# Kernel optimization log

Hardware: AMD Instinct MI355X
Metric: run time of the kernel (lower is better)

The kernel has to match this reference:

```python
import jax, jax.numpy as jnp
import numpy as np

ENC_STRIDES = [1, 2, 4, 8, 16, 32, 64, 128]
POST_STRIDES = [1, 2, 4, 8, 16, 32]
NHEAD = 4
EPS = 1e-5


def _fsmn(x, lw, lb, mw, mb, stride):
    # h = Linear(x); memory[i] = MemLinear(mean(x[:, max(0,i-stride):i+1]))
    # Sliding-window mean via cumsum trick (vectorizes the per-timestep loop).
    h = x @ lw.T + lb
    L = x.shape[1]
    cs = jnp.cumsum(x, axis=1)                                   # [B,L,D]
    cs0 = jnp.concatenate([jnp.zeros_like(cs[:, :1]), cs], axis=1)  # [B,L+1,D]
    idx = jnp.arange(L)
    start = jnp.maximum(0, idx - stride)
    counts = (idx + 1 - start).astype(x.dtype)
    means = (cs - cs0[:, start]) / counts[None, :, None]
    return h + means @ mw.T + mb


def _ln(x, w, b):
    m = x.mean(-1, keepdims=True)
    v = ((x - m) ** 2).mean(-1, keepdims=True)
    return (x - m) / jnp.sqrt(v + EPS) * w + b


def _mha(x, in_w, in_b, out_w, out_b):
    B, L, D = x.shape
    hd = D // NHEAD
    qkv = x @ in_w.T + in_b                       # [B,L,3D]
    q, k, v = jnp.split(qkv, 3, axis=-1)
    sp = lambda t: t.reshape(B, L, NHEAD, hd).transpose(0, 2, 1, 3)
    q, k, v = sp(q), sp(k), sp(v)
    scores = jnp.einsum('bhld,bhmd->bhlm', q, k) / jnp.sqrt(jnp.asarray(hd, x.dtype))
    att = jax.nn.softmax(scores, axis=-1)
    o = jnp.einsum('bhlm,bhmd->bhld', att, v).transpose(0, 2, 1, 3).reshape(B, L, D)
    return o @ out_w.T + out_b


def _forward(x, speaker_embeddings,
             enc0_in_w, enc0_in_b, enc_lin_w, enc_lin_b, enc_mem_w, enc_mem_b,
             spk_w1, spk_b1, spk_w2, spk_b2, spk_w3, spk_b3,
             tr_in_w, tr_in_b, tr_out_w, tr_out_b, tr_ln1_w, tr_ln1_b,
             tr_ff1_w, tr_ff1_b, tr_ff2_w, tr_ff2_b, tr_ln2_w, tr_ln2_b,
             adapter_w, adapter_b, post_lin_w, post_lin_b, post_mem_w, post_mem_b,
             cls_w1, cls_b1, cls_w2, cls_b2):
    # speech encoder: 8 FSMN layers (layer 0 has an input projection 80->512)
    h = x @ enc0_in_w.T + enc0_in_b
    for i in range(8):
        h = _fsmn(h, enc_lin_w[i], enc_lin_b[i], enc_mem_w[i], enc_mem_b[i], ENC_STRIDES[i])
    # speaker encoder MLP (dropout = identity in eval)
    sf = jax.nn.relu(speaker_embeddings @ spk_w1.T + spk_b1)
    sf = jax.nn.relu(sf @ spk_w2.T + spk_b2)
    sf = sf @ spk_w3.T + spk_b3                   # [B,S,D]
    # context-independent scores: [B,L,S]
    ci = jnp.einsum('bld,bsd->bls', h, sf)
    # context-dependent scorer: 4-layer post-norm transformer encoder (relu FFN)
    cd = h
    for i in range(4):
        a = _mha(cd, tr_in_w[i], tr_in_b[i], tr_out_w[i], tr_out_b[i])
        cd = _ln(cd + a, tr_ln1_w[i], tr_ln1_b[i])
        f = jax.nn.relu(cd @ tr_ff1_w[i].T + tr_ff1_b[i]) @ tr_ff2_w[i].T + tr_ff2_b[i]
        cd = _ln(cd + f, tr_ln2_w[i], tr_ln2_b[i])
    comb = jnp.concatenate([ci, cd], axis=2) @ adapter_w.T + adapter_b  # [B,L,D]
    for i in range(6):
        comb = _fsmn(comb, post_lin_w[i], post_lin_b[i], post_mem_w[i], post_mem_b[i], POST_STRIDES[i])
    out = jax.nn.relu(comb @ cls_w1.T + cls_b1) @ cls_w2.T + cls_b2
    return out


def setup_inputs() -> dict:
    B, L, F, D, S, C = 8, 2048, 80, 512, 4, 16
    key = jax.random.key(0)
    ks = iter(jax.random.split(key, 64))
    p = lambda shape, s=0.02: jax.random.normal(next(ks), shape, jnp.float32) * s
    inp = {
        'x': jax.random.normal(next(ks), (B, L, F), jnp.float32),
        'speaker_embeddings': jax.random.normal(next(ks), (B, S, 192), jnp.float32),
        'enc0_in_w': p((D, F)), 'enc0_in_b': p((D,)),
        'enc_lin_w': p((8, D, D)), 'enc_lin_b': p((8, D)),
        'enc_mem_w': p((8, D, D)), 'enc_mem_b': p((8, D)),
        'spk_w1': p((D, 192)), 'spk_b1': p((D,)),
        'spk_w2': p((D, D)), 'spk_b2': p((D,)),
        'spk_w3': p((D, D)), 'spk_b3': p((D,)),
        'tr_in_w': p((4, 3 * D, D)), 'tr_in_b': p((4, 3 * D)),
        'tr_out_w': p((4, D, D)), 'tr_out_b': p((4, D)),
        'tr_ln1_w': jnp.ones((4, D), jnp.float32), 'tr_ln1_b': jnp.zeros((4, D), jnp.float32),
        'tr_ff1_w': p((4, 4 * D, D)), 'tr_ff1_b': p((4, 4 * D)),
        'tr_ff2_w': p((4, D, 4 * D)), 'tr_ff2_b': p((4, D)),
        'tr_ln2_w': jnp.ones((4, D), jnp.float32), 'tr_ln2_b': jnp.zeros((4, D), jnp.float32),
        'adapter_w': p((D, S + D)), 'adapter_b': p((D,)),
        'post_lin_w': p((6, D, D)), 'post_lin_b': p((6, D)),
        'post_mem_w': p((6, D, D)), 'post_mem_b': p((6, D)),
        'cls_w1': p((D, D)), 'cls_b1': p((D,)),
        'cls_w2': p((C, D)), 'cls_b2': p((C,)),
    }
    return inp


def reference(x, speaker_embeddings,
              enc0_in_w, enc0_in_b, enc_lin_w, enc_lin_b, enc_mem_w, enc_mem_b,
              spk_w1, spk_b1, spk_w2, spk_b2, spk_w3, spk_b3,
              tr_in_w, tr_in_b, tr_out_w, tr_out_b, tr_ln1_w, tr_ln1_b,
              tr_ff1_w, tr_ff1_b, tr_ff2_w, tr_ff2_b, tr_ln2_w, tr_ln2_b,
              adapter_w, adapter_b, post_lin_w, post_lin_b, post_mem_w, post_mem_b,
              cls_w1, cls_b1, cls_w2, cls_b2):
    return _forward(x, speaker_embeddings,
                    enc0_in_w, enc0_in_b, enc_lin_w, enc_lin_b, enc_mem_w, enc_mem_b,
                    spk_w1, spk_b1, spk_w2, spk_b2, spk_w3, spk_b3,
                    tr_in_w, tr_in_b, tr_out_w, tr_out_b, tr_ln1_w, tr_ln1_b,
                    tr_ff1_w, tr_ff1_b, tr_ff2_w, tr_ff2_b, tr_ln2_w, tr_ln2_b,
                    adapter_w, adapter_b, post_lin_w, post_lin_b, post_mem_w, post_mem_b,
                    cls_w1, cls_b1, cls_w2, cls_b2)
```

## Files before the change

kernel.cpp:

```cpp
#include <hip/hip_runtime.h>
#include <hip/hip_bf16.h>
#include <math.h>

typedef unsigned short u16t;
using f32x4 = __attribute__((ext_vector_type(4))) float;
using s16x8 = __attribute__((ext_vector_type(8))) short;
using us8   = __attribute__((ext_vector_type(8))) unsigned short;

#define GB_RELU 1
#define GB_WF32 4
#define GB_WB16 8

__device__ __forceinline__ u16t f2b(float f) {
    unsigned u = __float_as_uint(f);
    unsigned r = (u + 0x7FFFu + ((u >> 16) & 1u)) >> 16;
    return (u16t)r;
}
__device__ __forceinline__ float b2f(u16t s) {
    return __uint_as_float(((unsigned)s) << 16);
}
__device__ __forceinline__ void gload16(const void* gsrc, void* ldst) {
    __builtin_amdgcn_global_load_lds(
        (const __attribute__((address_space(1))) void*)gsrc,
        (__attribute__((address_space(3))) void*)ldst, 16, 0, 0);
}

__global__ __launch_bounds__(512)
void gemm_bf16(const u16t* __restrict__ A, int lda,
               const u16t* __restrict__ W, int ldw,
               const float* __restrict__ bias,
               float* __restrict__ C, int ldc,
               u16t* __restrict__ Cb, int ldcb,
               int M, int N, int K, int flags)
{
    __shared__ u16t SM[32768];
    u16t* As = SM;
    u16t* Ws = SM + 16384;
    const int tid = threadIdx.x;
    const int lane = tid & 63, w = tid >> 6;
    const int wr = w >> 2, wc = w & 3;
    const int l15 = lane & 15, l4 = lane >> 4;

    unsigned nwg = gridDim.x * gridDim.y;
    unsigned bid = blockIdx.y * gridDim.x + blockIdx.x;
    if ((nwg & 7u) == 0u) bid = (bid & 7u) * (nwg >> 3) + (bid >> 3);
    const int m0 = (int)(bid / gridDim.x) * 128;
    const int n0 = (int)(bid % gridDim.x) * 128;

    int arow[2], wrow[2], koff[2], se0[2];
#pragma unroll
    for (int it = 0; it < 2; ++it) {
        const int e = it * 512 + tid;
        se0[it] = it * 512 + (tid & 448);
        const int kb = e >> 7, r = e & 127;
        const int rg = r ^ (kb & 3);
        int gm = m0 + rg; if (gm > M - 1) gm = M - 1;
        arow[it] = gm;
        wrow[it] = n0 + rg;
        koff[it] = kb * 8;
    }

    f32x4 acc[4][2];
#pragma unroll
    for (int i = 0; i < 4; ++i)
#pragma unroll
        for (int j = 0; j < 2; ++j) acc[i][j] = (f32x4){0.f, 0.f, 0.f, 0.f};

    auto STAGE = [&](int buf, int k0) {
#pragma unroll
        for (int it = 0; it < 2; ++it)
            gload16(A + (size_t)arow[it] * lda + k0 + koff[it],
                    &As[(size_t)(buf * 8192 + se0[it] * 8)]);
#pragma unroll
        for (int it = 0; it < 2; ++it)
            gload16(W + (size_t)wrow[it] * ldw + k0 + koff[it],
                    &Ws[(size_t)(buf * 8192 + se0[it] * 8)]);
    };

    const int nk = K >> 6;
    STAGE(0, 0);
    for (int ks = 0; ks < nk; ++ks) {
        const int cur = ks & 1;
        if (ks + 1 < nk) {
            STAGE(cur ^ 1, (ks + 1) << 6);
            asm volatile("s_waitcnt vmcnt(4)" ::: "memory");
        } else {
            asm volatile("s_waitcnt vmcnt(0)" ::: "memory");
        }
        __builtin_amdgcn_s_barrier();
#pragma unroll
        for (int kk = 0; kk < 2; ++kk) {
            const int kb = kk * 4 + l4;
            const int ls = l15 ^ l4;
            s16x8 a[4], b[2];
#pragma unroll
            for (int mi = 0; mi < 4; ++mi)
                a[mi] = *(const s16x8*)&As[(size_t)(cur * 8192 + (kb * 128 + wr * 64 + mi * 16 + ls) * 8)];
#pragma unroll
            for (int ni = 0; ni < 2; ++ni)
                b[ni] = *(const s16x8*)&Ws[(size_t)(cur * 8192 + (kb * 128 + wc * 32 + ni * 16 + ls) * 8)];
#pragma unroll
            for (int mi = 0; mi < 4; ++mi)
#pragma unroll
                for (int ni = 0; ni < 2; ++ni)
                    acc[mi][ni] = __builtin_amdgcn_mfma_f32_16x16x32_bf16(
                        a[mi], b[ni], acc[mi][ni], 0, 0, 0);
        }
        __builtin_amdgcn_s_barrier();
    }

    if (flags & GB_WB16) __syncthreads();
#pragma unroll
    for (int mi = 0; mi < 4; ++mi) {
#pragma unroll
        for (int r = 0; r < 4; ++r) {
            const int rowl = wr * 64 + mi * 16 + l4 * 4 + r;
            const int row = m0 + rowl;
            const bool rok = row < M;
#pragma unroll
            for (int ni = 0; ni < 2; ++ni) {
                const int coll = wc * 32 + ni * 16 + l15;
                float v = acc[mi][ni][r];
                if (bias) v += bias[n0 + coll];
                if (flags & GB_RELU) v = fmaxf(v, 0.f);
                if ((flags & GB_WF32) && rok) C[(size_t)row * ldc + n0 + coll] = v;
                if (flags & GB_WB16) SM[rowl * 136 + coll] = f2b(v);
            }
        }
    }
    if (flags & GB_WB16) {
        __syncthreads();
#pragma unroll
        for (int rr = 0; rr < 4; ++rr) {
            const int rowl = rr * 32 + (tid >> 4);
            const int c0 = (tid & 15) * 8;
            if (m0 + rowl < M)
                *(us8*)(Cb + (size_t)(m0 + rowl) * ldcb + n0 + c0) =
                    *(const us8*)&SM[rowl * 136 + c0];
        }
    }
}

__global__ __launch_bounds__(256)
void fsmn_means_b(u16t* __restrict__ HM, int stride)
{
    const int d = blockIdx.x * 256 + threadIdx.x;
    const int b = blockIdx.z;
    const int c0 = blockIdx.y * 128;
    const u16t* Hp = HM + (size_t)b * 2048 * 1024 + d;
    u16t* Mp = HM + (size_t)b * 2048 * 1024 + 512 + d;
    float sum = 0.f;
    int s0 = c0 - stride; if (s0 < 0) s0 = 0;
    for (int j = s0; j < c0; ++j) sum += b2f(Hp[(size_t)j * 1024]);
    for (int i = c0; i < c0 + 128; ++i) {
        sum += b2f(Hp[(size_t)i * 1024]);
        const int st = i - stride;
        const float cnt = (float)(i + 1 - (st > 0 ? st : 0));
        Mp[(size_t)i * 1024] = f2b(sum / cnt);
        if (st >= 0) sum -= b2f(Hp[(size_t)st * 1024]);
    }
}

__global__ __launch_bounds__(256)
void ci_kernel(const u16t* __restrict__ HM, const float* __restrict__ SF,
               float* __restrict__ CI)
{
    const int idx = blockIdx.x * 256 + threadIdx.x;
    const int s = idx & 3;
    const int bl = idx >> 2;
    const int b = bl >> 11;
    const us8* h8 = (const us8*)(HM + (size_t)bl * 1024);
    const float4* f4 = (const float4*)(SF + ((size_t)(b * 4 + s)) * 512);
    float acc = 0.f;
    for (int k = 0; k < 64; ++k) {
        const us8 hv = h8[k];
        const float4 f0 = f4[k * 2], f1 = f4[k * 2 + 1];
        acc += b2f(hv[0]) * f0.x + b2f(hv[1]) * f0.y + b2f(hv[2]) * f0.z + b2f(hv[3]) * f0.w
             + b2f(hv[4]) * f1.x + b2f(hv[5]) * f1.y + b2f(hv[6]) * f1.z + b2f(hv[7]) * f1.w;
    }
    CI[idx] = acc;
}

__global__ __launch_bounds__(256)
void ln_add_f32(const float* __restrict__ X, const float* __restrict__ R,
                const float* __restrict__ w, const float* __restrict__ b,
                float* __restrict__ Y, u16t* __restrict__ Yb)
{
    const int lane = threadIdx.x & 63, wid = threadIdx.x >> 6;
    const size_t row = (size_t)blockIdx.x * 4 + wid;
    const float* x = X + row * 512;
    const float* r = R + row * 512;
    const int c0 = lane * 8;
    float v[8];
    {
        const float4 a0 = *(const float4*)(x + c0);
        const float4 a1 = *(const float4*)(x + c0 + 4);
        const float4 r0 = *(const float4*)(r + c0);
        const float4 r1 = *(const float4*)(r + c0 + 4);
        v[0] = a0.x + r0.x; v[1] = a0.y + r0.y; v[2] = a0.z + r0.z; v[3] = a0.w + r0.w;
        v[4] = a1.x + r1.x; v[5] = a1.y + r1.y; v[6] = a1.z + r1.z; v[7] = a1.w + r1.w;
    }
    float s = 0.f;
#pragma unroll
    for (int j = 0; j < 8; ++j) s += v[j];
#pragma unroll
    for (int off = 1; off < 64; off <<= 1) s += __shfl_xor(s, off);
    const float mean = s * (1.f / 512.f);
    float q = 0.f;
#pragma unroll
    for (int j = 0; j < 8; ++j) { const float dd = v[j] - mean; q += dd * dd; }
#pragma unroll
    for (int off = 1; off < 64; off <<= 1) q += __shfl_xor(q, off);
    const float rstd = rsqrtf(q * (1.f / 512.f) + 1e-5f);
    float* y = Y + row * 512;
    u16t* yb = Yb + row * 1024;
#pragma unroll
    for (int j = 0; j < 8; ++j) {
        const float o = (v[j] - mean) * rstd * w[c0 + j] + b[c0 + j];
        y[c0 + j] = o;
        yb[c0 + j] = f2b(o);
    }
}

__global__ __launch_bounds__(256)
void vtprep(const u16t* __restrict__ QKVb, u16t* __restrict__ Vt)
{
    __shared__ u16t T[128 * 72];
    const int tid = threadIdx.x;
    const int l0 = blockIdx.x * 64;
    const int bh = blockIdx.y, b = bh >> 2, h = bh & 3;
#pragma unroll
    for (int it = 0; it < 4; ++it) {
        const int e = it * 256 + tid;
        const int l = e >> 4, dc = e & 15;
        const us8 v = *(const us8*)(QKVb + ((size_t)(b * 2048 + l0 + l)) * 1536
                                   + 1024 + h * 128 + dc * 8);
#pragma unroll
        for (int j = 0; j < 8; ++j) T[(dc * 8 + j) * 72 + l] = v[j];
    }
    __syncthreads();
#pragma unroll
    for (int it = 0; it < 4; ++it) {
        const int e = it * 256 + tid;
        const int d = e >> 3, lc = e & 7;
        const us8 ov = *(const us8*)&T[d * 72 + lc * 8];
        *(us8*)(Vt + ((size_t)bh * 128 + d) * 2048 + l0 + lc * 8) = ov;
    }
}

__global__ __launch_bounds__(512)
void attn_bf16(const u16t* __restrict__ QKVb, const u16t* __restrict__ Vt,
               u16t* __restrict__ AOb)
{
    __shared__ u16t Kt[2][8192];
    __shared__ u16t Vtl[2][8192];
    __shared__ u16t Pl[8192];
    const int tid = threadIdx.x, lane = tid & 63, w = tid >> 6;
    const int l15 = lane & 15, l4 = lane >> 4;
    const unsigned bid = blockIdx.y * gridDim.x + blockIdx.x;
    const int xcd = bid & 7, idx = bid >> 3;
    const int bh = xcd * 4 + (idx & 3);
    const int q0 = (idx >> 2) * 128;
    const int b = bh >> 2, h = bh & 3;
    const float SCALE = 0.08838834764831845f;

    int krow[2], kdoff[2], vd[2], vkoff[2], se0[2];
#pragma unroll
    for (int it = 0; it < 2; ++it) {
        const int e = it * 512 + tid;
        se0[it] = it * 512 + (tid & 448);
        const int dblk = e >> 6, key = e & 63;
        krow[it] = key ^ (dblk & 3);
        kdoff[it] = dblk * 8;
        const int kb = e >> 7, d = e & 127;
        vd[it] = d ^ (kb & 3);
        vkoff[it] = kb * 8;
    }
    auto STAGE = [&](int buf, int k0) {
#pragma unroll
        for (int it = 0; it < 2; ++it)
            gload16(QKVb + ((size_t)(b * 2048 + k0 + krow[it])) * 1536 + 512 + h * 128 + kdoff[it],
                    &Kt[buf][(size_t)se0[it] * 8]);
#pragma unroll
        for (int it = 0; it < 2; ++it)
            gload16(Vt + ((size_t)bh * 128 + vd[it]) * 2048 + k0 + vkoff[it],
                    &Vtl[buf][(size_t)se0[it] * 8]);
    };

    s16x8 qf[4];
    {
        const u16t* qp = QKVb + ((size_t)(b * 2048 + q0 + w * 16 + l15)) * 1536
                         + h * 128 + l4 * 8;
#pragma unroll
        for (int ks = 0; ks < 4; ++ks) qf[ks] = *(const s16x8*)(qp + ks * 32);
    }
    asm volatile("s_waitcnt vmcnt(0)" ::: "memory");

    f32x4 o[8];
#pragma unroll
    for (int i = 0; i < 8; ++i) o[i] = (f32x4){0.f, 0.f, 0.f, 0.f};
    f32x4 m_run, lsum;
#pragma unroll
    for (int r = 0; r < 4; ++r) { m_run[r] = -1e30f; lsum[r] = 0.f; }

    const int ls = l15 ^ l4;
    STAGE(0, 0);
    for (int kt = 0; kt < 32; ++kt) {
        const int cur = kt & 1;
        if (kt + 1 < 32) {
            STAGE(cur ^ 1, (kt + 1) * 64);
            asm volatile("s_waitcnt vmcnt(4)" ::: "memory");
        } else {
            asm volatile("s_waitcnt vmcnt(0)" ::: "memory");
        }
        __builtin_amdgcn_s_barrier();

        f32x4 s[4];
#pragma unroll
        for (int ni = 0; ni < 4; ++ni) s[ni] = (f32x4){0.f, 0.f, 0.f, 0.f};
#pragma unroll
        for (int ks = 0; ks < 4; ++ks) {
#pragma unroll
            for (int ni = 0; ni < 4; ++ni) {
                const s16x8 kf = *(const s16x8*)&Kt[cur][(size_t)((ks * 4 + l4) * 64 + ni * 16 + ls) * 8];
                s[ni] = __builtin_amdgcn_mfma_f32_16x16x32_bf16(qf[ks], kf, s[ni], 0, 0, 0);
            }
        }
        f32x4 mx;
#pragma unroll
        for (int r = 0; r < 4; ++r)
            mx[r] = fmaxf(fmaxf(s[0][r], s[1][r]), fmaxf(s[2][r], s[3][r])) * SCALE;
#pragma unroll
        for (int off = 1; off < 16; off <<= 1)
#pragma unroll
            for (int r = 0; r < 4; ++r) mx[r] = fmaxf(mx[r], __shfl_xor(mx[r], off));
        bool small = true;
#pragma unroll
        for (int r = 0; r < 4; ++r) small = small && (mx[r] <= m_run[r] + 8.f);
        if (!__all(small)) {
            f32x4 corr;
#pragma unroll
            for (int r = 0; r < 4; ++r) {
                const float nm = fmaxf(m_run[r], mx[r]);
                corr[r] = __expf(m_run[r] - nm);
                m_run[r] = nm;
                lsum[r] *= corr[r];
            }
#pragma unroll
            for (int ni = 0; ni < 8; ++ni)
#pragma unroll
                for (int r = 0; r < 4; ++r) o[ni][r] *= corr[r];
        }
        float p[4][4];
#pragma unroll
        for (int ni = 0; ni < 4; ++ni)
#pragma unroll
            for (int r = 0; r < 4; ++r) {
                p[ni][r] = __expf(s[ni][r] * SCALE - m_run[r]);
                lsum[r] += p[ni][r];
            }
#pragma unroll
        for (int ni = 0; ni < 4; ++ni) {
            const int key = ni * 16 + l15;
            const int kb = key >> 3, kj = key & 7;
#pragma unroll
            for (int r = 0; r < 4; ++r)
                Pl[(size_t)((w * 8 + kb) * 16 + l4 * 4 + r) * 8 + kj] = f2b(p[ni][r]);
        }
#pragma unroll
        for (int kk = 0; kk < 2; ++kk) {
            const s16x8 pa = *(const s16x8*)&Pl[(size_t)((w * 8 + kk * 4 + l4) * 16 + l15) * 8];
#pragma unroll
            for (int ni = 0; ni < 8; ++ni) {
                const s16x8 vf = *(const s16x8*)&Vtl[cur][(size_t)((kk * 4 + l4) * 128 + ni * 16 + ls) * 8];
                o[ni] = __builtin_amdgcn_mfma_f32_16x16x32_bf16(pa, vf, o[ni], 0, 0, 0);
            }
        }
        __builtin_amdgcn_s_barrier();
    }
#pragma unroll
    for (int off = 1; off < 16; off <<= 1)
#pragma unroll
        for (int r = 0; r < 4; ++r) lsum[r] += __shfl_xor(lsum[r], off);
    f32x4 inv;
#pragma unroll
    for (int r = 0; r < 4; ++r) inv[r] = 1.f / lsum[r];
#pragma unroll
    for (int ni = 0; ni < 8; ++ni)
#pragma unroll
        for (int r = 0; r < 4; ++r)
            AOb[((size_t)(b * 2048 + q0 + w * 16 + l4 * 4 + r)) * 512
                + h * 128 + ni * 16 + l15] = f2b(o[ni][r] * inv[r]);
}

__global__ __launch_bounds__(256)
void concat_b(const float* __restrict__ CI, const u16t* __restrict__ HM,
              u16t* __restrict__ OUTC)
{
    const size_t total = (size_t)16384 * 576;
    size_t i = (size_t)blockIdx.x * 256 + threadIdx.x;
    if (i >= total) return;
    const int col = (int)(i % 576);
    const size_t rowi = i / 576;
    u16t v = 0;
    if (col < 4) v = f2b(CI[rowi * 4 + col]);
    else if (col < 516) v = HM[rowi * 1024 + (col - 4)];
    OUTC[i] = v;
}

__global__ __launch_bounds__(256)
void cvt_plain(const float* __restrict__ src, u16t* __restrict__ dst, size_t n8)
{
    const size_t i = (size_t)blockIdx.x * 256 + threadIdx.x;
    if (i >= n8) return;
    const float4 a = ((const float4*)src)[i * 2];
    const float4 b = ((const float4*)src)[i * 2 + 1];
    us8 o;
    o[0] = f2b(a.x); o[1] = f2b(a.y); o[2] = f2b(a.z); o[3] = f2b(a.w);
    o[4] = f2b(b.x); o[5] = f2b(b.y); o[6] = f2b(b.z); o[7] = f2b(b.w);
    ((us8*)dst)[i] = o;
}

__global__ __launch_bounds__(256)
void cvt_pad(const float* __restrict__ src, u16t* __restrict__ dst,
             int rows, int sc, int dc)
{
    const size_t i = (size_t)blockIdx.x * 256 + threadIdx.x;
    const size_t total = (size_t)rows * dc;
    if (i >= total) return;
    const int c = (int)(i % dc);
    const size_t r = i / dc;
    dst[i] = (c < sc) ? f2b(src[r * sc + c]) : (u16t)0;
}

__global__ __launch_bounds__(256)
void cvt_fuse(const float* __restrict__ lsrc, const float* __restrict__ msrc,
              u16t* __restrict__ dst, int n)
{
    const int idx = blockIdx.x * 256 + threadIdx.x;
    if (idx >= n) return;
    const int k = idx & 511;
    const int nn = (idx >> 9) & 511;
    const int i = idx >> 18;
    const size_t base = (size_t)i * 524288 + (size_t)nn * 1024 + k;
    dst[base] = f2b(lsrc[idx]);
    dst[base + 512] = f2b(msrc[idx]);
}

__global__ __launch_bounds__(256)
void bias_fuse(const float* __restrict__ a, const float* __restrict__ b,
               float* __restrict__ dst, int n)
{
    const int i = blockIdx.x * 256 + threadIdx.x;
    if (i < n) dst[i] = a[i] + b[i];
}

__global__ __launch_bounds__(256)
void cls2_kernel(const float* __restrict__ T1, const float* __restrict__ W2,
                 const float* __restrict__ b2, float* __restrict__ out)
{
    const int t = threadIdx.x;
    const int r = blockIdx.x * 16 + (t >> 4), c = t & 15;
    const float4* a = (const float4*)(T1 + (size_t)r * 512);
    const float4* wv = (const float4*)(W2 + (size_t)c * 512);
    float acc = 0.f;
    for (int k = 0; k < 128; ++k) {
        const float4 x = a[k], y = wv[k];
        acc += x.x * y.x + x.y * y.y + x.z * y.z + x.w * y.w;
    }
    out[(size_t)r * 16 + c] = acc + b2[c];
}

extern "C" void kernel_launch(void* const* d_in, const int* in_sizes, int n_in,
                              void* d_out, int out_size, void* d_ws, size_t ws_size,
                              hipStream_t stream)
{
    (void)in_sizes; (void)n_in; (void)out_size; (void)ws_size;
    const int M = 16384;

    const float* x        = (const float*)d_in[0];
    const float* spk_emb  = (const float*)d_in[1];
    const float* enc0_w   = (const float*)d_in[2];
    const float* enc0_b   = (const float*)d_in[3];
    const float* enc_lw   = (const float*)d_in[4];
    const float* enc_lb   = (const float*)d_in[5];
    const float* enc_mw   = (const float*)d_in[6];
    const float* enc_mb   = (const float*)d_in[7];
    const float* spk_w1   = (const float*)d_in[8];
    const float* spk_b1   = (const float*)d_in[9];
    const float* spk_w2   = (const float*)d_in[10];
    const float* spk_b2   = (const float*)d_in[11];
    const float* spk_w3   = (const float*)d_in[12];
    const float* spk_b3   = (const float*)d_in[13];
    const float* tr_in_w  = (const float*)d_in[14];
    const float* tr_in_b  = (const float*)d_in[15];
    const float* tr_out_w = (const float*)d_in[16];
    const float* tr_out_b = (const float*)d_in[17];
    const float* tr_ln1_w = (const float*)d_in[18];
    const float* tr_ln1_b = (const float*)d_in[19];
    const float* tr_ff1_w = (const float*)d_in[20];
    const float* tr_ff1_b = (const float*)d_in[21];
    const float* tr_ff2_w = (const float*)d_in[22];
    const float* tr_ff2_b = (const float*)d_in[23];
    const float* tr_ln2_w = (const float*)d_in[24];
    const float* tr_ln2_b = (const float*)d_in[25];
    const float* adpt_w   = (const float*)d_in[26];
    const float* adpt_b   = (const float*)d_in[27];
    const float* post_lw  = (const float*)d_in[28];
    const float* post_lb  = (const float*)d_in[29];
    const float* post_mw  = (const float*)d_in[30];
    const float* post_mb  = (const float*)d_in[31];
    const float* cls_w1   = (const float*)d_in[32];
    const float* cls_b1   = (const float*)d_in[33];
    const float* cls_w2   = (const float*)d_in[34];
    const float* cls_b2   = (const float*)d_in[35];

    char* wsp = (char*)d_ws;
    size_t off = 0;
    auto alloc = [&](size_t bytes) -> void* {
        void* p = wsp + off; off += (bytes + 255) & ~(size_t)255; return p;
    };
    float* H    = (float*)alloc((size_t)M * 512 * 4);
    float* T1   = (float*)alloc((size_t)M * 512 * 4);
    u16t*  HM0  = (u16t*) alloc((size_t)M * 1024 * 2);
    u16t*  AOb  = (u16t*) alloc((size_t)M * 512 * 2);
    u16t*  BIG  = (u16t*) alloc((size_t)M * 2048 * 2);
    float* CI   = (float*)alloc((size_t)M * 4 * 4);
    float* S3   = (float*)alloc(32 * 512 * 4);
    u16t* enc0_wb   = (u16t*)alloc(512 * 128 * 2);
    u16t* encFW     = (u16t*)alloc((size_t)8 * 512 * 1024 * 2);
    float* encFB    = (float*)alloc(8 * 512 * 4);
    u16t* spk_embb  = (u16t*)alloc(32 * 192 * 2);
    u16t* spk_w1b   = (u16t*)alloc(512 * 192 * 2);
    u16t* spk_w2b   = (u16t*)alloc(512 * 512 * 2);
    u16t* spk_w3b   = (u16t*)alloc(512 * 512 * 2);
    u16t* tr_in_wb  = (u16t*)alloc((size_t)4 * 1536 * 512 * 2);
    u16t* tr_out_wb = (u16t*)alloc((size_t)4 * 512 * 512 * 2);
    u16t* tr_ff1_wb = (u16t*)alloc((size_t)4 * 2048 * 512 * 2);
    u16t* tr_ff2_wb = (u16t*)alloc((size_t)4 * 2048 * 512 * 2);
    u16t* adpt_wb   = (u16t*)alloc(512 * 576 * 2);
    u16t* postFW    = (u16t*)alloc((size_t)6 * 512 * 1024 * 2);
    float* postFB   = (float*)alloc(6 * 512 * 4);
    u16t* cls_w1b   = (u16t*)alloc(512 * 512 * 2);
    u16t* S1b       = (u16t*)alloc(32 * 512 * 2);
    u16t* S2b       = (u16t*)alloc(32 * 512 * 2);

    u16t* HM1   = BIG;
    u16t* xb    = BIG;
    u16t* QKVb  = BIG;
    u16t* Vt    = BIG + (size_t)M * 1536;
    u16t* Fb    = BIG;
    u16t* Xcatb = BIG;
    u16t* HMs[2] = {HM0, HM1};

    auto cplain = [&](const float* s, u16t* d, size_t n) {
        const size_t n8 = n / 8;
        cvt_plain<<<dim3((unsigned)((n8 + 255) / 256)), dim3(256), 0, stream>>>(s, d, n8);
    };
    auto cpad = [&](const float* s, u16t* d, int rows, int sc, int dc) {
        const size_t tot = (size_t)rows * dc;
        cvt_pad<<<dim3((unsigned)((tot + 255) / 256)), dim3(256), 0, stream>>>(s, d, rows, sc, dc);
    };
    auto gemm = [&](const u16t* A, int lda, const u16t* W, int ldw,
                    const float* bias, float* C, int ldc, u16t* Cb, int ldcb,
                    int m, int n, int k, int flags) {
        dim3 g(n / 128, (m + 127) / 128);
        gemm_bf16<<<g, dim3(512), 0, stream>>>(A, lda, W, ldw, bias,
                                               C, ldc, Cb, ldcb, m, n, k, flags);
    };

    cpad(x, xb, M, 80, 128);
    cpad(enc0_w, enc0_wb, 512, 80, 128);
    cvt_fuse<<<dim3(2097152 / 256), dim3(256), 0, stream>>>(enc_lw, enc_mw, encFW, 2097152);
    bias_fuse<<<dim3(16), dim3(256), 0, stream>>>(enc_lb, enc_mb, encFB, 4096);
    cplain(spk_emb, spk_embb, 32 * 192);
    cplain(spk_w1, spk_w1b, 512 * 192);
    cplain(spk_w2, spk_w2b, 512 * 512);
    cplain(spk_w3, spk_w3b, 512 * 512);
    cplain(tr_in_w, tr_in_wb, (size_t)4 * 1536 * 512);
    cplain(tr_out_w, tr_out_wb, (size_t)4 * 512 * 512);
    cplain(tr_ff1_w, tr_ff1_wb, (size_t)4 * 2048 * 512);
    cplain(tr_ff2_w, tr_ff2_wb, (size_t)4 * 2048 * 512);
    cpad(adpt_w, adpt_wb, 512, 516, 576);
    cvt_fuse<<<dim3(1572864 / 256), dim3(256), 0, stream>>>(post_lw, post_mw, postFW, 1572864);
    bias_fuse<<<dim3(12), dim3(256), 0, stream>>>(post_lb, post_mb, postFB, 3072);
    cplain(cls_w1, cls_w1b, 512 * 512);

    gemm(xb, 128, enc0_wb, 128, enc0_b,
         nullptr, 0, HM0, 1024, M, 512, 128, GB_WB16);
    for (int i = 0; i < 8; ++i) {
        u16t* src = HMs[i & 1];
        u16t* dst = HMs[(i + 1) & 1];
        fsmn_means_b<<<dim3(2, 16, 8), dim3(256), 0, stream>>>(src, 1 << i);
        gemm(src, 1024, encFW + (size_t)i * 524288, 1024, encFB + (size_t)i * 512,
             (i == 7 ? H : nullptr), 512, dst, 1024, M, 512, 1024,
             GB_WB16 | (i == 7 ? GB_WF32 : 0));
    }

    gemm(spk_embb, 192, spk_w1b, 192, spk_b1,
         nullptr, 0, S1b, 512, 32, 512, 192, GB_RELU | GB_WB16);
    gemm(S1b, 512, spk_w2b, 512, spk_b2,
         nullptr, 0, S2b, 512, 32, 512, 512, GB_RELU | GB_WB16);
    gemm(S2b, 512, spk_w3b, 512, spk_b3,
         S3, 512, nullptr, 0, 32, 512, 512, GB_WF32);

    ci_kernel<<<dim3(65536 / 256), dim3(256), 0, stream>>>(HM0, S3, CI);

    for (int i = 0; i < 4; ++i) {
        gemm(HM0, 1024, tr_in_wb + (size_t)i * 786432, 512, tr_in_b + (size_t)i * 1536,
             nullptr, 0, QKVb, 1536, M, 1536, 512, GB_WB16);
        vtprep<<<dim3(32, 32), dim3(256), 0, stream>>>(QKVb, Vt);
        attn_bf16<<<dim3(16, 32), dim3(512), 0, stream>>>(QKVb, Vt, AOb);
        gemm(AOb, 512, tr_out_wb + (size_t)i * 262144, 512, tr_out_b + (size_t)i * 512,
             T1, 512, nullptr, 0, M, 512, 512, GB_WF32);
        ln_add_f32<<<dim3(M / 4), dim3(256), 0, stream>>>(
            H, T1, tr_ln1_w + (size_t)i * 512, tr_ln1_b + (size_t)i * 512, H, HM0);
        gemm(HM0, 1024, tr_ff1_wb + (size_t)i * 1048576, 512, tr_ff1_b + (size_t)i * 2048,
             nullptr, 0, Fb, 2048, M, 2048, 512, GB_RELU | GB_WB16);
        gemm(Fb, 2048, tr_ff2_wb + (size_t)i * 1048576, 2048, tr_ff2_b + (size_t)i * 512,
             T1, 512, nullptr, 0, M, 512, 2048, GB_WF32);
        ln_add_f32<<<dim3(M / 4), dim3(256), 0, stream>>>(
            H, T1, tr_ln2_w + (size_t)i * 512, tr_ln2_b + (size_t)i * 512, H, HM0);
    }

    concat_b<<<dim3((unsigned)(((size_t)M * 576 + 255) / 256)), dim3(256), 0, stream>>>(CI, HM0, Xcatb);
    gemm(Xcatb, 576, adpt_wb, 576, adpt_b,
         nullptr, 0, HM0, 1024, M, 512, 576, GB_WB16);

    for (int i = 0; i < 6; ++i) {
        u16t* src = HMs[i & 1];
        u16t* dst = HMs[(i + 1) & 1];
        fsmn_means_b<<<dim3(2, 16, 8), dim3(256), 0, stream>>>(src, 1 << i);
        gemm(src, 1024, postFW + (size_t)i * 524288, 1024, postFB + (size_t)i * 512,
             nullptr, 0, dst, 1024, M, 512, 1024, GB_WB16);
    }

    gemm(HM0, 1024, cls_w1b, 512, cls_b1,
         T1, 512, nullptr, 0, M, 512, 512, GB_RELU | GB_WF32);
    cls2_kernel<<<dim3(M / 16), dim3(256), 0, stream>>>(T1, cls_w2, cls_b2, (float*)d_out);
}
```

Baseline: 3.500 ms.

## Fuse V transpose into QKV GEMM, bf16 residuals, exp2 softmax, new pipelining

The QKV projection GEMM now writes the V columns straight into the transposed Vt layout, which removes the separate vtprep kernel. The out-proj and FF2 GEMMs write bf16 instead of fp32, and ln_add reads that bf16 residual, halving intermediate traffic at some cost in precision. In attention, the scale is folded into a log2 factor for exp2f, and the online-softmax rescale check is done per element without a max reduction. The GEMM and attention loops switch from vmcnt(4) double-buffer waits to a full wait plus __syncthreads at the end of each step, which may reduce load/compute overlap.

```diff
diff --git a/kernel.cpp b/kernel.cpp
--- a/kernel.cpp
+++ b/kernel.cpp
@@ -10,6 +10,7 @@
 #define GB_RELU 1
 #define GB_WF32 4
 #define GB_WB16 8
+#define GB_WVT  16
 
 __device__ __forceinline__ u16t f2b(float f) {
     unsigned u = __float_as_uint(f);
@@ -31,6 +32,7 @@
                const float* __restrict__ bias,
                float* __restrict__ C, int ldc,
                u16t* __restrict__ Cb, int ldcb,
+               u16t* __restrict__ VT,
                int M, int N, int K, int flags)
 {
     __shared__ u16t SM[32768];
@@ -79,15 +81,11 @@
 
     const int nk = K >> 6;
     STAGE(0, 0);
+    asm volatile("s_waitcnt vmcnt(0)" ::: "memory");
+    __syncthreads();
+    int cur = 0;
     for (int ks = 0; ks < nk; ++ks) {
-        const int cur = ks & 1;
-        if (ks + 1 < nk) {
-            STAGE(cur ^ 1, (ks + 1) << 6);
-            asm volatile("s_waitcnt vmcnt(4)" ::: "memory");
-        } else {
-            asm volatile("s_waitcnt vmcnt(0)" ::: "memory");
-        }
-        __builtin_amdgcn_s_barrier();
+        if (ks + 1 < nk) STAGE(cur ^ 1, (ks + 1) << 6);
 #pragma unroll
         for (int kk = 0; kk < 2; ++kk) {
             const int kb = kk * 4 + l4;
@@ -106,37 +104,70 @@
                     acc[mi][ni] = __builtin_amdgcn_mfma_f32_16x16x32_bf16(
                         a[mi], b[ni], acc[mi][ni], 0, 0, 0);
         }
-        __builtin_amdgcn_s_barrier();
-    }
-
+        if (ks + 1 < nk) {
+            asm volatile("s_waitcnt vmcnt(0)" ::: "memory");
+            __syncthreads();
+            cur ^= 1;
+        }
+    }
+
+    const bool isVT = (flags & GB_WVT) && (n0 >= 1024);
     if (flags & GB_WB16) __syncthreads();
-#pragma unroll
-    for (int mi = 0; mi < 4; ++mi) {
-#pragma unroll
-        for (int r = 0; r < 4; ++r) {
-            const int rowl = wr * 64 + mi * 16 + l4 * 4 + r;
-            const int row = m0 + rowl;
-            const bool rok = row < M;
-#pragma unroll
-            for (int ni = 0; ni < 2; ++ni) {
-                const int coll = wc * 32 + ni * 16 + l15;
-                float v = acc[mi][ni][r];
-                if (bias) v += bias[n0 + coll];
-                if (flags & GB_RELU) v = fmaxf(v, 0.f);
-                if ((flags & GB_WF32) && rok) C[(size_t)row * ldc + n0 + coll] = v;
-                if (flags & GB_WB16) SM[rowl * 136 + coll] = f2b(v);
+    if (isVT) {
+        const int bb = m0 >> 11, l0 = m0 & 2047;
+        const int h = (n0 - 1024) >> 7;
+        const int bh = bb * 4 + h;
+#pragma unroll
+        for (int mi = 0; mi < 4; ++mi) {
+#pragma unroll
+            for (int r = 0; r < 4; ++r) {
+                const int rowl = wr * 64 + mi * 16 + l4 * 4 + r;
+#pragma unroll
+                for (int ni = 0; ni < 2; ++ni) {
+                    const int coll = wc * 32 + ni * 16 + l15;
+                    float v = acc[mi][ni][r];
+                    if (bias) v += bias[n0 + coll];
+                    SM[coll * 136 + rowl] = f2b(v);
+                }
             }
         }
-    }
-    if (flags & GB_WB16) {
         __syncthreads();
 #pragma unroll
-        for (int rr = 0; rr < 4; ++rr) {
-            const int rowl = rr * 32 + (tid >> 4);
-            const int c0 = (tid & 15) * 8;
-            if (m0 + rowl < M)
-                *(us8*)(Cb + (size_t)(m0 + rowl) * ldcb + n0 + c0) =
-                    *(const us8*)&SM[rowl * 136 + c0];
+        for (int it = 0; it < 4; ++it) {
+            const int idx = it * 512 + tid;
+            const int d = idx >> 4, rblk = idx & 15;
+            *(us8*)(VT + ((size_t)(bh * 128 + d)) * 2048 + l0 + rblk * 8) =
+                *(const us8*)&SM[d * 136 + rblk * 8];
+        }
+    } else {
+#pragma unroll
+        for (int mi = 0; mi < 4; ++mi) {
+#pragma unroll
+            for (int r = 0; r < 4; ++r) {
+                const int rowl = wr * 64 + mi * 16 + l4 * 4 + r;
+                const int row = m0 + rowl;
+                const bool rok = row < M;
+#pragma unroll
+                for (int ni = 0; ni < 2; ++ni) {
+                    const int coll = wc * 32 + ni * 16 + l15;
+                    float v = acc[mi][ni][r];
+                    if (bias) v += bias[n0 + coll];
+                    if (flags & GB_RELU) v = fmaxf(v, 0.f);
+                    if ((flags & GB_WF32) && rok) C[(size_t)row * ldc + n0 + coll] = v;
+                    if (flags & GB_WB16) SM[rowl * 136 + coll] = f2b(v);
+                }
+            }
+        }
+        if (flags & GB_WB16) {
+            __syncthreads();
+#pragma unroll
+            for (int rr = 0; rr < 4; ++rr) {
+                const int rowl = rr * 32 + (tid >> 4);
+                const int c0 = (tid & 15) * 8;
+                if (m0 + rowl < M)
+                    *(us8*)(Cb + (size_t)(m0 + rowl) * ldcb + n0 + c0) =
+                        *(const us8*)&SM[rowl * 136 + c0];
+            }
         }
     }
 }
@@ -182,23 +213,24 @@
 }
 
 __global__ __launch_bounds__(256)
-void ln_add_f32(const float* __restrict__ X, const float* __restrict__ R,
+void ln_add_f32(const float* __restrict__ X, const u16t* __restrict__ Rb,
                 const float* __restrict__ w, const float* __restrict__ b,
                 float* __restrict__ Y, u16t* __restrict__ Yb)
 {
     const int lane = threadIdx.x & 63, wid = threadIdx.x >> 6;
     const size_t row = (size_t)blockIdx.x * 4 + wid;
     const float* x = X + row * 512;
-    const float* r = R + row * 512;
+    const u16t* r = Rb + row * 512;
     const int c0 = lane * 8;
     float v[8];
     {
         const float4 a0 = *(const float4*)(x + c0);
         const float4 a1 = *(const float4*)(x + c0 + 4);
-        const float4 r0 = *(const float4*)(r + c0);
-        const float4 r1 = *(const float4*)(r + c0 + 4);
-        v[0] = a0.x + r0.x; v[1] = a0.y + r0.y; v[2] = a0.z + r0.z; v[3] = a0.w + r0.w;
-        v[4] = a1.x + r1.x; v[5] = a1.y + r1.y; v[6] = a1.z + r1.z; v[7] = a1.w + r1.w;
+        const us8 r8 = *(const us8*)(r + c0);
+        v[0] = a0.x + b2f(r8[0]); v[1] = a0.y + b2f(r8[1]);
+        v[2] = a0.z + b2f(r8[2]); v[3] = a0.w + b2f(r8[3]);
+        v[4] = a1.x + b2f(r8[4]); v[5] = a1.y + b2f(r8[5]);
+        v[6] = a1.z + b2f(r8[6]); v[7] = a1.w + b2f(r8[7]);
     }
     float s = 0.f;
 #pragma unroll
@@ -219,32 +251,6 @@
         const float o = (v[j] - mean) * rstd * w[c0 + j] + b[c0 + j];
         y[c0 + j] = o;
         yb[c0 + j] = f2b(o);
-    }
-}
-
-__global__ __launch_bounds__(256)
-void vtprep(const u16t* __restrict__ QKVb, u16t* __restrict__ Vt)
-{
-    __shared__ u16t T[128 * 72];
-    const int tid = threadIdx.x;
-    const int l0 = blockIdx.x * 64;
-    const int bh = blockIdx.y, b = bh >> 2, h = bh & 3;
-#pragma unroll
-    for (int it = 0; it < 4; ++it) {
-        const int e = it * 256 + tid;
-        const int l = e >> 4, dc = e & 15;
-        const us8 v = *(const us8*)(QKVb + ((size_t)(b * 2048 + l0 + l)) * 1536
-                                   + 1024 + h * 128 + dc * 8);
-#pragma unroll
-        for (int j = 0; j < 8; ++j) T[(dc * 8 + j) * 72 + l] = v[j];
-    }
-    __syncthreads();
-#pragma unroll
-    for (int it = 0; it < 4; ++it) {
-        const int e = it * 256 + tid;
-        const int d = e >> 3, lc = e & 7;
-        const us8 ov = *(const us8*)&T[d * 72 + lc * 8];
-        *(us8*)(Vt + ((size_t)bh * 128 + d) * 2048 + l0 + lc * 8) = ov;
     }
 }
 
@@ -262,7 +268,8 @@
     const int bh = xcd * 4 + (idx & 3);
     const int q0 = (idx >> 2) * 128;
     const int b = bh >> 2, h = bh & 3;
-    const float SCALE = 0.08838834764831845f;
+    const float S2 = 0.12751744f;
+    const float THR2 = 11.5415603f;
 
     int krow[2], kdoff[2], vd[2], vkoff[2], se0[2];
 #pragma unroll
@@ -294,7 +301,9 @@
 #pragma unroll
         for (int ks = 0; ks < 4; ++ks) qf[ks] = *(const s16x8*)(qp + ks * 32);
     }
+    STAGE(0, 0);
     asm volatile("s_waitcnt vmcnt(0)" ::: "memory");
+    __syncthreads();
 
     f32x4 o[8];
 #pragma unroll
@@ -304,16 +313,9 @@
     for (int r = 0; r < 4; ++r) { m_run[r] = -1e30f; lsum[r] = 0.f; }
 
     const int ls = l15 ^ l4;
-    STAGE(0, 0);
+    int cur = 0;
     for (int kt = 0; kt < 32; ++kt) {
-        const int cur = kt & 1;
-        if (kt + 1 < 32) {
-            STAGE(cur ^ 1, (kt + 1) * 64);
-            asm volatile("s_waitcnt vmcnt(4)" ::: "memory");
-        } else {
-            asm volatile("s_waitcnt vmcnt(0)" ::: "memory");
-        }
-        __builtin_amdgcn_s_barrier();
+        if (kt + 1 < 32) STAGE(cur ^ 1, (kt + 1) * 64);
 
         f32x4 s[4];
 #pragma unroll
@@ -326,23 +328,30 @@
                 s[ni] = __builtin_amdgcn_mfma_f32_16x16x32_bf16(qf[ks], kf, s[ni], 0, 0, 0);
             }
         }
-        f32x4 mx;
-#pragma unroll
-        for (int r = 0; r < 4; ++r)
-            mx[r] = fmaxf(fmaxf(s[0][r], s[1][r]), fmaxf(s[2][r], s[3][r])) * SCALE;
-#pragma unroll
-        for (int off = 1; off < 16; off <<= 1)
-#pragma unroll
-            for (int r = 0; r < 4; ++r) mx[r] = fmaxf(mx[r], __shfl_xor(mx[r], off));
-        bool small = true;
-#pragma unroll
-        for (int r = 0; r < 4; ++r) small = small && (mx[r] <= m_run[r] + 8.f);
-        if (!__all(small)) {
+#pragma unroll
+        for (int ni = 0; ni < 4; ++ni)
+#pragma unroll
+            for (int r = 0; r < 4; ++r) s[ni][r] *= S2;
+
+        bool ok = true;
+#pragma unroll
+        for (int ni = 0; ni < 4; ++ni)
+#pragma unroll
+            for (int r = 0; r < 4; ++r) ok = ok && (s[ni][r] <= m_run[r] + THR2);
+        if (!__all(ok)) {
+            f32x4 mx;
+#pragma unroll
+            for (int r = 0; r < 4; ++r)
+                mx[r] = fmaxf(fmaxf(s[0][r], s[1][r]), fmaxf(s[2][r], s[3][r]));
+#pragma unroll
+            for (int off = 1; off < 16; off <<= 1)
+#pragma unroll
+                for (int r = 0; r < 4; ++r) mx[r] = fmaxf(mx[r], __shfl_xor(mx[r], off));
             f32x4 corr;
 #pragma unroll
             for (int r = 0; r < 4; ++r) {
                 const float nm = fmaxf(m_run[r], mx[r]);
-                corr[r] = __expf(m_run[r] - nm);
+                corr[r] = exp2f(m_run[r] - nm);
                 m_run[r] = nm;
                 lsum[r] *= corr[r];
             }
@@ -356,7 +365,7 @@
         for (int ni = 0; ni < 4; ++ni)
 #pragma unroll
             for (int r = 0; r < 4; ++r) {
-                p[ni][r] = __expf(s[ni][r] * SCALE - m_run[r]);
+                p[ni][r] = exp2f(s[ni][r] - m_run[r]);
                 lsum[r] += p[ni][r];
             }
 #pragma unroll
@@ -376,7 +385,11 @@
                 o[ni] = __builtin_amdgcn_mfma_f32_16x16x32_bf16(pa, vf, o[ni], 0, 0, 0);
             }
         }
-        __builtin_amdgcn_s_barrier();
+        if (kt + 1 < 32) {
+            asm volatile("s_waitcnt vmcnt(0)" ::: "memory");
+            __syncthreads();
+            cur ^= 1;
+        }
     }
 #pragma unroll
     for (int off = 1; off < 16; off <<= 1)
@@ -551,6 +564,7 @@
     u16t* Vt    = BIG + (size_t)M * 1536;
     u16t* Fb    = BIG;
     u16t* Xcatb = BIG;
+    u16t* T1b   = (u16t*)T1;
     u16t* HMs[2] = {HM0, HM1};
 
     auto cplain = [&](const float* s, u16t* d, size_t n) {
@@ -563,10 +577,10 @@
     };
     auto gemm = [&](const u16t* A, int lda, const u16t* W, int ldw,
                     const float* bias, float* C, int ldc, u16t* Cb, int ldcb,
-                    int m, int n, int k, int flags) {
+                    u16t* VT, int m, int n, int k, int flags) {
         dim3 g(n / 128, (m + 127) / 128);
         gemm_bf16<<<g, dim3(512), 0, stream>>>(A, lda, W, ldw, bias,
-                                               C, ldc, Cb, ldcb, m, n, k, flags);
+                                               C, ldc, Cb, ldcb, VT, m, n, k, flags);
     };
 
     cpad(x, xb, M, 80, 128);
@@ -587,55 +601,54 @@
     cplain(cls_w1, cls_w1b, 512 * 512);
 
     gemm(xb, 128, enc0_wb, 128, enc0_b,
-         nullptr, 0, HM0, 1024, M, 512, 128, GB_WB16);
+         nullptr, 0, HM0, 1024, nullptr, M, 512, 128, GB_WB16);
     for (int i = 0; i < 8; ++i) {
         u16t* src = HMs[i & 1];
         u16t* dst = HMs[(i + 1) & 1];
         fsmn_means_b<<<dim3(2, 16, 8), dim3(256), 0, stream>>>(src, 1 << i);
         gemm(src, 1024, encFW + (size_t)i * 524288, 1024, encFB + (size_t)i * 512,
-             (i == 7 ? H : nullptr), 512, dst, 1024, M, 512, 1024,
+             (i == 7 ? H : nullptr), 512, dst, 1024, nullptr, M, 512, 1024,
              GB_WB16 | (i == 7 ? GB_WF32 : 0));
     }
 
     gemm(spk_embb, 192, spk_w1b, 192, spk_b1,
-         nullptr, 0, S1b, 512, 32, 512, 192, GB_RELU | GB_WB16);
+         nullptr, 0, S1b, 512, nullptr, 32, 512, 192, GB_RELU | GB_WB16);
     gemm(S1b, 512, spk_w2b, 512, spk_b2,
-         nullptr, 0, S2b, 512, 32, 512, 512, GB_RELU | GB_WB16);
+         nullptr, 0, S2b, 512, nullptr, 32, 512, 512, GB_RELU | GB_WB16);
     gemm(S2b, 512, spk_w3b, 512, spk_b3,
-         S3, 512, nullptr, 0, 32, 512, 512, GB_WF32);
+         S3, 512, nullptr, 0, nullptr, 32, 512, 512, GB_WF32);
 
     ci_kernel<<<dim3(65536 / 256), dim3(256), 0, stream>>>(HM0, S3, CI);
 
     for (int i = 0; i < 4; ++i) {
         gemm(HM0, 1024, tr_in_wb + (size_t)i * 786432, 512, tr_in_b + (size_t)i * 1536,
-             nullptr, 0, QKVb, 1536, M, 1536, 512, GB_WB16);
-        vtprep<<<dim3(32, 32), dim3(256), 0, stream>>>(QKVb, Vt);
+             nullptr, 0, QKVb, 1536, Vt, M, 1536, 512, GB_WB16 | GB_WVT);
         attn_bf16<<<dim3(16, 32), dim3(512), 0, stream>>>(QKVb, Vt, AOb);
         gemm(AOb, 512, tr_out_wb + (size_t)i * 262144, 512, tr_out_b + (size_t)i * 512,
-             T1, 512, nullptr, 0, M, 512, 512, GB_WF32);
+             nullptr, 0, T1b, 512, nullptr, M, 512, 512, GB_WB16);
         ln_add_f32<<<dim3(M / 4), dim3(256), 0, stream>>>(
-            H, T1, tr_ln1_w + (size_t)i * 512, tr_ln1_b + (size_t)i * 512, H, HM0);
+            H, T1b, tr_ln1_w + (size_t)i * 512, tr_ln1_b + (size_t)i * 512, H, HM0);
         gemm(HM0, 1024, tr_ff1_wb + (size_t)i * 1048576, 512, tr_ff1_b + (size_t)i * 2048,
-             nullptr, 0, Fb, 2048, M, 2048, 512, GB_RELU | GB_WB16);
+             nullptr, 0, Fb, 2048, nullptr, M, 2048, 512, GB_RELU | GB_WB16);
         gemm(Fb, 2048, tr_ff2_wb + (size_t)i * 1048576, 2048, tr_ff2_b + (size_t)i * 512,
-             T1, 512, nullptr, 0, M, 512, 2048, GB_WF32);
+             nullptr, 0, T1b, 512, nullptr, M, 512, 2048, GB_WB16);
         ln_add_f32<<<dim3(M / 4), dim3(256), 0, stream>>>(
-            H, T1, tr_ln2_w + (size_t)i * 512, tr_ln2_b + (size_t)i * 512, H, HM0);
+            H, T1b, tr_ln2_w + (size_t)i * 512, tr_ln2_b + (size_t)i * 512, H, HM0);
     }
 
     concat_b<<<dim3((unsigned)(((size_t)M * 576 + 255) / 256)), dim3(256), 0, stream>>>(CI, HM0, Xcatb);
     gemm(Xcatb, 576, adpt_wb, 576, adpt_b,
-         nullptr, 0, HM0, 1024, M, 512, 576, GB_WB16);
+         nullptr, 0, HM0, 1024, nullptr, M, 512, 576, GB_WB16);
 
     for (int i = 0; i < 6; ++i) {
         u16t* src = HMs[i & 1];
         u16t* dst = HMs[(i + 1) & 1];
         fsmn_means_b<<<dim3(2, 16, 8), dim3(256), 0, stream>>>(src, 1 << i);
         gemm(src, 1024, postFW + (size_t)i * 524288, 1024, postFB + (size_t)i * 512,
-             nullptr, 0, dst, 1024, M, 512, 1024, GB_WB16);
+             nullptr, 0, dst, 1024, nullptr, M, 512, 1024, GB_WB16);
     }
 
     gemm(HM0, 1024, cls_w1b, 512, cls_b1,
-         T1, 512, nullptr, 0, M, 512, 512, GB_RELU | GB_WF32);
+         T1, 512, nullptr, 0, nullptr, M, 512, 512, GB_RELU | GB_WF32);
     cls2_kernel<<<dim3(M / 16), dim3(256), 0, stream>>>(T1, cls_w2, cls_b2, (float*)d_out);
 }
```

Result: slower. 3.761 ms (+7.5%).
